# Kernel tuning notes

Measured on AMD Instinct MI355X. Metric: run time of the kernel, lower is better.

Reference implementation:

```python
import jax, jax.numpy as jnp
import numpy as np

MESH_POS = jnp.array([0.0, 0.0, -0.8], dtype=jnp.float32)
CAMERA_F = (248.0, 248.0)
CAMERA_C = (111.5, 111.5)


def _camera_mat(p):
    # p: [B, 5] camera metadata (azimuth deg, elevation deg, _, distance, _)
    d = jnp.pi / 180.0
    theta = p[:, 0] * d
    camy = p[:, 3] * jnp.sin(p[:, 1] * d)
    lens = p[:, 3] * jnp.cos(p[:, 1] * d)
    camx = lens * jnp.cos(theta)
    camz = lens * jnp.sin(theta)
    Z = jnp.stack([camx, camy, camz], -1)  # camera origin [B,3]
    Y = jnp.stack([camy * jnp.cos(theta + jnp.pi), lens,
                   camy * jnp.sin(theta + jnp.pi)], -1)
    X = jnp.cross(Y, Z)
    nrm = lambda v: v / jnp.linalg.norm(v, axis=-1, keepdims=True)
    cm = jnp.stack([nrm(X), nrm(Y), nrm(Z)], -2)  # [B,3,3] orthonormal rows
    return cm, Z


def _camera_trans(p, xyz):  # world -> camera: (xyz - O) @ cm.T
    cm, o = _camera_mat(p)
    return jnp.einsum('bij,bnj->bni', cm, xyz - o[:, None, :])


def _camera_trans_inv(p, xyz):  # camera -> world; cm orthonormal so inv(cm) = cm.T
    cm, o = _camera_mat(p)
    return jnp.einsum('bnj,bji->bni', xyz, cm) + o[:, None, :]


def _grid_sample(feat, gx, gy):
    # torch F.grid_sample: bilinear, padding_mode='zeros', align_corners=False
    B, C, H, W = feat.shape
    x = ((gx + 1.0) * W - 1.0) * 0.5  # [B,N] pixel coords
    y = ((gy + 1.0) * H - 1.0) * 0.5
    x0, y0 = jnp.floor(x), jnp.floor(y)
    x1, y1 = x0 + 1.0, y0 + 1.0
    wx1, wy1 = x - x0, y - y0
    wx0, wy0 = 1.0 - wx1, 1.0 - wy1
    flat = feat.reshape(B, C, H * W)

    def corner(xc, yc, wgt):
        xi = jnp.clip(xc, 0, W - 1).astype(jnp.int32)
        yi = jnp.clip(yc, 0, H - 1).astype(jnp.int32)
        valid = (xc >= 0) & (xc <= W - 1) & (yc >= 0) & (yc <= H - 1)
        v = jnp.take_along_axis(flat, (yi * W + xi)[:, None, :], axis=2)  # [B,C,N]
        return v * (wgt * valid)[:, None, :]

    out = (corner(x0, y0, wx0 * wy0) + corner(x1, y0, wx1 * wy0)
           + corner(x0, y1, wx0 * wy1) + corner(x1, y1, wx1 * wy1))
    return out.transpose(0, 2, 1)  # [B,N,C]


def setup_inputs() -> dict:
    key = jax.random.key(0)
    ks = jax.random.split(key, 7)
    B, V, N = 8, 3, 8192
    feat0 = jax.random.normal(ks[0], (V, B, 64, 56, 56), jnp.float32)
    feat1 = jax.random.normal(ks[1], (V, B, 128, 28, 28), jnp.float32)
    feat2 = jax.random.normal(ks[2], (V, B, 256, 14, 14), jnp.float32)
    inputs = jax.random.normal(ks[3], (B, N, 3), jnp.float32) * 0.2
    az = jax.random.uniform(ks[4], (B, V), minval=0.0, maxval=360.0)
    el = jax.random.uniform(ks[5], (B, V), minval=20.0, maxval=40.0)
    dist = jax.random.uniform(ks[6], (B, V), minval=0.8, maxval=1.2)
    poses = jnp.stack([az, el, jnp.zeros((B, V)), dist,
                       jnp.full((B, V), 25.0)], axis=-1).astype(jnp.float32)
    resolution = jnp.full((2,), 224, dtype=jnp.int32)
    return {"feat0": feat0, "feat1": feat1, "feat2": feat2,
            "inputs": inputs, "poses": poses, "resolution": resolution}


def reference(feat0, feat1, feat2, inputs, poses, resolution):
    res = resolution.astype(jnp.float32)
    half_res = (res - 1.0) * 0.5
    c_off0 = CAMERA_C[0] - half_res[0]
    c_off1 = CAMERA_C[1] - half_res[1]
    positions = inputs + MESH_POS
    point_origin = _camera_trans_inv(poses[:, 0], positions)
    V = poses.shape[1]
    feats_views = []
    for i in range(V):  # small fixed view count
        pos = _camera_trans(poses[:, i], point_origin)
        X, Y, Z = pos[..., 0], pos[..., 1], pos[..., 2]
        w = -CAMERA_F[0] * (X / Z) + c_off0  # bound=0 -> bound_val is identity
        h = CAMERA_F[1] * (Y / Z) + c_off1
        w = jnp.clip(w / half_res[0], -1.0, 1.0)
        h = jnp.clip(h / half_res[1], -1.0, 1.0)
        f = jnp.concatenate([_grid_sample(feat0[i], w, h),
                             _grid_sample(feat1[i], w, h),
                             _grid_sample(feat2[i], w, h)], axis=2)
        feats_views.append(f)
    outputs = jnp.stack(feats_views, axis=1)  # [B,V,N,448]
    out_max = jnp.max(outputs, axis=1)
    out_mean = jnp.mean(outputs, axis=1)
    out_std = jnp.std(outputs, axis=1, ddof=1)  # torch.std is unbiased
    return jnp.concatenate([inputs, out_max, out_mean, out_std], axis=2)
```

## Files before the change

### kernel.cpp

```cpp
#include <hip/hip_runtime.h>
#include <cstdint>
#include <cmath>


typedef float f32x2 __attribute__((ext_vector_type(2)));
typedef float f32x4 __attribute__((ext_vector_type(4)));
typedef _Float16 f16;
typedef _Float16 f16x2 __attribute__((ext_vector_type(2)));
typedef _Float16 f16x4 __attribute__((ext_vector_type(4)));

__device__ __forceinline__ void make_cam(const float* __restrict__ p, float* c) {
    const float d = 0.017453292519943295f;
    float theta = p[0] * d;
    float elr   = p[1] * d;
    float dist  = p[3];
    float st = sinf(theta), ct = cosf(theta);
    float se = sinf(elr),   ce = cosf(elr);
    float camy = dist * se;
    float lens = dist * ce;
    float camx = lens * ct;
    float camz = lens * st;
    float Zx = camx, Zy = camy, Zz = camz;
    float Yx = -camy * ct, Yy = lens, Yz = -camy * st;
    float Xx = Yy * Zz - Yz * Zy;
    float Xy = Yz * Zx - Yx * Zz;
    float Xz = Yx * Zy - Yy * Zx;
    float rx = 1.0f / sqrtf(Xx*Xx + Xy*Xy + Xz*Xz);
    float ry = 1.0f / sqrtf(Yx*Yx + Yy*Yy + Yz*Yz);
    float rz = 1.0f / sqrtf(Zx*Zx + Zy*Zy + Zz*Zz);
    c[0] = Xx*rx; c[1] = Xy*rx; c[2] = Xz*rx;
    c[3] = Yx*ry; c[4] = Yy*ry; c[5] = Yz*ry;
    c[6] = Zx*rz; c[7] = Zy*rz; c[8] = Zz*rz;
    c[9] = camx; c[10] = camy; c[11] = camz;
}

__global__ void setup_cams_kernel(const float* __restrict__ poses,
                                  const int* __restrict__ resolution,
                                  float* __restrict__ ws, int BV) {
    int t = blockIdx.x * blockDim.x + threadIdx.x;
    if (t == 0) {
        float h0 = ((float)resolution[0] - 1.0f) * 0.5f;
        float h1 = ((float)resolution[1] - 1.0f) * 0.5f;
        ws[0] = 111.5f - h0;
        ws[1] = 111.5f - h1;
        ws[2] = h0;
        ws[3] = h1;
    }
    if (t < BV) make_cam(poses + (size_t)t * 5, ws + 4 + (size_t)t * 12);
}

struct Corners {
    int p00, p10, p01, p11;
    float w00, w10, w01, w11;
};

__device__ __forceinline__ Corners mk_corners(float gx, float gy, int S) {
    float x = ((gx + 1.0f) * (float)S - 1.0f) * 0.5f;
    float y = ((gy + 1.0f) * (float)S - 1.0f) * 0.5f;
    float x0f = floorf(x), y0f = floorf(y);
    float wx1 = x - x0f, wy1 = y - y0f;
    float wx0 = 1.0f - wx1, wy0 = 1.0f - wy1;
    int x0 = (int)x0f, y0 = (int)y0f;
    int x1 = x0 + 1, y1 = y0 + 1;
    bool vx0 = (x0 >= 0) && (x0 <= S - 1);
    bool vx1 = (x1 >= 0) && (x1 <= S - 1);
    bool vy0 = (y0 >= 0) && (y0 <= S - 1);
    bool vy1 = (y1 >= 0) && (y1 <= S - 1);
    int xi0 = min(max(x0, 0), S - 1);
    int xi1 = min(max(x1, 0), S - 1);
    int yi0 = min(max(y0, 0), S - 1);
    int yi1 = min(max(y1, 0), S - 1);
    Corners c;
    c.p00 = yi0 * S + xi0;
    c.p10 = yi0 * S + xi1;
    c.p01 = yi1 * S + xi0;
    c.p11 = yi1 * S + xi1;
    c.w00 = wx0 * wy0 * ((vx0 && vy0) ? 1.0f : 0.0f);
    c.w10 = wx1 * wy0 * ((vx1 && vy0) ? 1.0f : 0.0f);
    c.w01 = wx0 * wy1 * ((vx0 && vy1) ? 1.0f : 0.0f);
    c.w11 = wx1 * wy1 * ((vx1 && vy1) ? 1.0f : 0.0f);
    return c;
}

__global__ __launch_bounds__(256) void prep_kernel(
    const float* __restrict__ f0, const float* __restrict__ f1,
    const float* __restrict__ f2, f16* __restrict__ t0, f16* __restrict__ t1,
    f16* __restrict__ t2, const float* __restrict__ inputs,
    const float* __restrict__ poses, const int* __restrict__ resolution,
    float* __restrict__ corn, int B, int N, int BV, int tgrid) {
    __shared__ float tile[32][33];
    const int bid = blockIdx.x;
    if (bid < tgrid) {
        const int nb0 = 98 * 2 * BV;
        const int nb1 = 25 * 4 * BV;
        const float* src; f16* dst; int C, P, tP, local;
        if (bid < nb0)            { src = f0; dst = t0; C = 64;  P = 3136; tP = 98; local = bid; }
        else if (bid < nb0 + nb1) { src = f1; dst = t1; C = 128; P = 784;  tP = 25; local = bid - nb0; }
        else                      { src = f2; dst = t2; C = 256; P = 196;  tP = 7;  local = bid - nb0 - nb1; }
        int per = tP * (C >> 5);
        int slice = local / per;
        int rem = local - slice * per;
        int cy = rem / tP;
        int cx = rem - cy * tP;
        const float* s = src + (size_t)slice * C * P;
        f16* d = dst + (size_t)slice * C * P;
        int p0 = cx * 32, c0 = cy * 32;
        int tx = threadIdx.x & 31, ty = threadIdx.x >> 5;
#pragma unroll
        for (int i = 0; i < 32; i += 8) {
            int c = c0 + ty + i, p = p0 + tx;
            if (p < P) tile[ty + i][tx] = s[(size_t)c * P + p];
        }
        __syncthreads();
#pragma unroll
        for (int i = 0; i < 32; i += 8) {
            int p = p0 + ty + i, c = c0 + tx;
            if (p < P) d[(size_t)p * C + c] = (f16)tile[tx][ty + i];
        }
    } else {
        int t = (bid - tgrid) * 256 + threadIdx.x;
        if (t >= B * N * 3) return;
        int point = t / 3;
        int v = t - point * 3;
        int b = point / N;

        float h0 = ((float)resolution[0] - 1.0f) * 0.5f;
        float h1 = ((float)resolution[1] - 1.0f) * 0.5f;
        float c_off0 = 111.5f - h0, c_off1 = 111.5f - h1;
        float inv_h0 = 1.0f / h0, inv_h1 = 1.0f / h1;

        float cm0[12], cmv[12];
        make_cam(poses + (size_t)(b * 3) * 5, cm0);
        make_cam(poses + (size_t)(b * 3 + v) * 5, cmv);

        const float* ip = inputs + (size_t)point * 3;
        const float px = ip[0], py = ip[1], pz = ip[2] - 0.8f;

        const float wx = px * cm0[0] + py * cm0[3] + pz * cm0[6] + cm0[9];
        const float wy = px * cm0[1] + py * cm0[4] + pz * cm0[7] + cm0[10];
        const float wz = px * cm0[2] + py * cm0[5] + pz * cm0[8] + cm0[11];

        float qx = wx - cmv[9], qy = wy - cmv[10], qz = wz - cmv[11];
        float Xc = cmv[0] * qx + cmv[1] * qy + cmv[2] * qz;
        float Yc = cmv[3] * qx + cmv[4] * qy + cmv[5] * qz;
        float Zc = cmv[6] * qx + cmv[7] * qy + cmv[8] * qz;
        float invZ = 1.0f / Zc;
        float wpix = -248.0f * (Xc * invZ) + c_off0;
        float hpix =  248.0f * (Yc * invZ) + c_off1;
        float gx = fminf(fmaxf(wpix * inv_h0, -1.0f), 1.0f);
        float gy = fminf(fmaxf(hpix * inv_h1, -1.0f), 1.0f);

        float* o = corn + (size_t)t * 24;
        const int S[3] = {56, 28, 14};
        const int CB[3] = {64 * 2, 128 * 2, 256 * 2};
#pragma unroll
        for (int lvl = 0; lvl < 3; ++lvl) {
            Corners cr = mk_corners(gx, gy, S[lvl]);
            o[lvl * 8 + 0] = __int_as_float(cr.p00 * CB[lvl]);
            o[lvl * 8 + 1] = __int_as_float(cr.p10 * CB[lvl]);
            o[lvl * 8 + 2] = __int_as_float(cr.p01 * CB[lvl]);
            o[lvl * 8 + 3] = __int_as_float(cr.p11 * CB[lvl]);
            o[lvl * 8 + 4] = cr.w00;
            o[lvl * 8 + 5] = cr.w10;
            o[lvl * 8 + 6] = cr.w01;
            o[lvl * 8 + 7] = cr.w11;
        }
    }
}

template <int VEC> struct VecOf;
template <> struct VecOf<1> { using T = float; };
template <> struct VecOf<2> { using T = f32x2; };
template <> struct VecOf<4> { using T = f32x4; };
template <int VEC> struct F16VecOf;
template <> struct F16VecOf<1> { using T = f16; };
template <> struct F16VecOf<2> { using T = f16x2; };
template <> struct F16VecOf<4> { using T = f16x4; };

template <int VEC>
__device__ __forceinline__ typename VecOf<VEC>::T
gather4(const f16* __restrict__ base, const int4 off, const float4 w, int lane) {
    using HV = typename F16VecOf<VEC>::T;
    using FV = typename VecOf<VEC>::T;
    const char* cb = (const char*)base;
    const int lo = lane * (VEC * 2);
    HV h00 = *(const HV*)(cb + off.x + lo);
    HV h10 = *(const HV*)(cb + off.y + lo);
    HV h01 = *(const HV*)(cb + off.z + lo);
    HV h11 = *(const HV*)(cb + off.w + lo);
    FV a00, a10, a01, a11;
    if constexpr (VEC == 1) {
        a00 = (float)h00; a10 = (float)h10; a01 = (float)h01; a11 = (float)h11;
    } else {
        a00 = __builtin_convertvector(h00, FV);
        a10 = __builtin_convertvector(h10, FV);
        a01 = __builtin_convertvector(h01, FV);
        a11 = __builtin_convertvector(h11, FV);
    }
    return w.x * a00 + w.y * a10 + w.z * a01 + w.w * a11;
}

template <typename VecT, int VEC>
__device__ __forceinline__ void stats3(VecT a, VecT b, VecT c,
                                       VecT* omx, VecT* ome, VecT* osd) {
    const float* pa = (const float*)&a;
    const float* pb = (const float*)&b;
    const float* pc = (const float*)&c;
    float* qx = (float*)omx; float* qe = (float*)ome; float* qs = (float*)osd;
#pragma unroll
    for (int j = 0; j < VEC; ++j) {
        float x = pa[j], y = pb[j], z = pc[j];
        float m = fmaxf(x, fmaxf(y, z));
        float mean = (x + y + z) * (1.0f / 3.0f);
        float dx = x - mean, dy = y - mean, dz = z - mean;
        float s = sqrtf((dx * dx + dy * dy + dz * dz) * 0.5f);
        qx[j] = m; qe[j] = mean; qs[j] = s;
    }
}

__global__ __launch_bounds__(256) void gproj_main_kernel(
    const f16* __restrict__ t0, const f16* __restrict__ t1,
    const f16* __restrict__ t2, const float* __restrict__ inputs,
    const float* __restrict__ corn, float* __restrict__ out, int B, int N) {
    __shared__ alignas(16) float sb[4 * 1347];
    const int wave = threadIdx.x >> 6;
    const int lane = threadIdx.x & 63;
    const int b = blockIdx.x % B;
    const int pb = (blockIdx.x / B) * 4;
    const int pib = pb + wave;
    const bool valid = pib < N;

    if (valid) {
        const int point = b * N + pib;
        const int pu = __builtin_amdgcn_readfirstlane(point);
        const int bu = __builtin_amdgcn_readfirstlane(b);
        const float* ip = inputs + (size_t)point * 3;

        float  v0[3];
        f32x2  v1[3];
        f32x4  v2[3];

#pragma unroll
        for (int v = 0; v < 3; ++v) {
            const float* cp = corn + (size_t)(pu * 3 + v) * 24;
            const int slice = v * B + bu;
            const f16* b0 = t0 + (size_t)slice * 64 * 3136;
            const f16* b1 = t1 + (size_t)slice * 128 * 784;
            const f16* b2 = t2 + (size_t)slice * 256 * 196;

            int4   o0 = *(const int4*)(cp);
            float4 w0 = *(const float4*)(cp + 4);
            int4   o1 = *(const int4*)(cp + 8);
            float4 w1 = *(const float4*)(cp + 12);
            int4   o2 = *(const int4*)(cp + 16);
            float4 w2 = *(const float4*)(cp + 20);

            v0[v] = gather4<1>(b0, o0, w0, lane);
            v1[v] = gather4<2>(b1, o1, w1, lane);
            v2[v] = gather4<4>(b2, o2, w2, lane);
        }

        float* row = sb + wave * 1347;
        if (lane < 3) row[lane] = ip[lane];
        {
            float mx = fmaxf(v0[0], fmaxf(v0[1], v0[2]));
            float mean = (v0[0] + v0[1] + v0[2]) * (1.0f / 3.0f);
            float dx = v0[0] - mean, dy = v0[1] - mean, dz = v0[2] - mean;
            float sd = sqrtf((dx * dx + dy * dy + dz * dz) * 0.5f);
            row[3 + lane] = mx;
            row[451 + lane] = mean;
            row[899 + lane] = sd;
        }
        {
            f32x2 mx, me, sd;
            stats3<f32x2, 2>(v1[0], v1[1], v1[2], &mx, &me, &sd);
            const int g = 64 + 2 * lane;
            row[3 + g] = mx.x;   row[3 + g + 1] = mx.y;
            row[451 + g] = me.x; row[451 + g + 1] = me.y;
            row[899 + g] = sd.x; row[899 + g + 1] = sd.y;
        }
        {
            f32x4 mx, me, sd;
            stats3<f32x4, 4>(v2[0], v2[1], v2[2], &mx, &me, &sd);
            const int g = 192 + 4 * lane;
#pragma unroll
            for (int e = 0; e < 4; ++e) {
                row[3 + g + e] = mx[e];
                row[451 + g + e] = me[e];
                row[899 + g + e] = sd[e];
            }
        }
    }
    __syncthreads();

    const int nvalid = min(N - pb, 4);
    const int len = nvalid * 1347;
    float* gout = out + (size_t)(b * N + pb) * 1347;
    const int len4 = len & ~3;
    for (int j = threadIdx.x * 4; j < len4; j += 1024) {
        f32x4 vv = *(const f32x4*)(sb + j);
        __builtin_nontemporal_store(vv, (f32x4*)(gout + j));
    }
    if ((len & 3) && threadIdx.x == 0) {
        for (int jj = len4; jj < len; ++jj) gout[jj] = sb[jj];
    }
}

template <int C, int VEC>
__device__ __forceinline__ typename VecOf<VEC>::T
samph(const f16* __restrict__ base, const Corners& cr, int lane) {
    using HV = typename F16VecOf<VEC>::T;
    using FV = typename VecOf<VEC>::T;
    const HV* r00 = (const HV*)(base + (size_t)cr.p00 * C);
    const HV* r10 = (const HV*)(base + (size_t)cr.p10 * C);
    const HV* r01 = (const HV*)(base + (size_t)cr.p01 * C);
    const HV* r11 = (const HV*)(base + (size_t)cr.p11 * C);
    HV h00 = r00[lane], h10 = r10[lane], h01 = r01[lane], h11 = r11[lane];
    FV a00, a10, a01, a11;
    if constexpr (VEC == 1) {
        a00 = (float)h00; a10 = (float)h10; a01 = (float)h01; a11 = (float)h11;
    } else {
        a00 = __builtin_convertvector(h00, FV);
        a10 = __builtin_convertvector(h10, FV);
        a01 = __builtin_convertvector(h01, FV);
        a11 = __builtin_convertvector(h11, FV);
    }
    return cr.w00 * a00 + cr.w10 * a10 + cr.w01 * a01 + cr.w11 * a11;
}

template <typename VecT, int VEC>
__device__ __forceinline__ void stats3_st(VecT a, VecT b, VecT c,
                                          float* pmx, float* pme, float* psd) {
    VecT mx, me, sd;
    stats3<VecT, VEC>(a, b, c, &mx, &me, &sd);
    *(VecT*)pmx = mx; *(VecT*)pme = me; *(VecT*)psd = sd;
}

__global__ __launch_bounds__(256) void gproj_fused_kernel(
    const f16* __restrict__ t0, const f16* __restrict__ t1,
    const f16* __restrict__ t2, const float* __restrict__ inputs,
    const float* __restrict__ cams, float* __restrict__ out, int B, int N) {
    const int wave = threadIdx.x >> 6;
    const int lane = threadIdx.x & 63;
    const int b = blockIdx.x % B;
    const int pib = (blockIdx.x / B) * 4 + wave;
    if (pib >= N) return;
    const int point = b * N + pib;

    const float c_off0 = cams[0], c_off1 = cams[1];
    const float inv_h0 = 1.0f / cams[2], inv_h1 = 1.0f / cams[3];
    const float* cam = cams + 4;

    const float* ip = inputs + (size_t)point * 3;
    const float px = ip[0], py = ip[1], pz = ip[2] - 0.8f;

    const float* m0 = cam + (size_t)(b * 3) * 12;
    const float wx = px * m0[0] + py * m0[3] + pz * m0[6] + m0[9];
    const float wy = px * m0[1] + py * m0[4] + pz * m0[7] + m0[10];
    const float wz = px * m0[2] + py * m0[5] + pz * m0[8] + m0[11];

    float  v0[3];
    f32x2  v1[3];
    f32x4  v2[3];

#pragma unroll
    for (int v = 0; v < 3; ++v) {
        const float* m = cam + (size_t)(b * 3 + v) * 12;
        float qx = wx - m[9], qy = wy - m[10], qz = wz - m[11];
        float Xc = m[0] * qx + m[1] * qy + m[2] * qz;
        float Yc = m[3] * qx + m[4] * qy + m[5] * qz;
        float Zc = m[6] * qx + m[7] * qy + m[8] * qz;
        float invZ = 1.0f / Zc;
        float wpix = -248.0f * (Xc * invZ) + c_off0;
        float hpix =  248.0f * (Yc * invZ) + c_off1;
        float gx = fminf(fmaxf(wpix * inv_h0, -1.0f), 1.0f);
        float gy = fminf(fmaxf(hpix * inv_h1, -1.0f), 1.0f);
        Corners cr0 = mk_corners(gx, gy, 56);
        Corners cr1 = mk_corners(gx, gy, 28);
        Corners cr2 = mk_corners(gx, gy, 14);
        const int slice = v * B + b;
        v0[v] = samph<64, 1>(t0 + (size_t)slice * 64 * 3136, cr0, lane);
        v1[v] = samph<128, 2>(t1 + (size_t)slice * 128 * 784, cr1, lane);
        v2[v] = samph<256, 4>(t2 + (size_t)slice * 256 * 196, cr2, lane);
    }

    float* op = out + (size_t)point * 1347;
    if (lane < 3) op[lane] = ip[lane];
    {
        float* basep = op + 3 + lane;
        float mx = fmaxf(v0[0], fmaxf(v0[1], v0[2]));
        float mean = (v0[0] + v0[1] + v0[2]) * (1.0f / 3.0f);
        float dx = v0[0] - mean, dy = v0[1] - mean, dz = v0[2] - mean;
        float sd = sqrtf((dx * dx + dy * dy + dz * dz) * 0.5f);
        basep[0] = mx; basep[448] = mean; basep[896] = sd;
    }
    {
        const int g = 64 + 2 * lane;
        stats3_st<f32x2, 2>(v1[0], v1[1], v1[2],
                            op + 3 + g, op + 451 + g, op + 899 + g);
    }
    {
        const int g = 192 + 4 * lane;
        stats3_st<f32x4, 4>(v2[0], v2[1], v2[2],
                            op + 3 + g, op + 451 + g, op + 899 + g);
    }
}

__device__ __forceinline__ float samp_cf(const float* __restrict__ base,
                                         const Corners& cr, int P, int c) {
    const float* bc = base + (size_t)c * P;
    return cr.w00 * bc[cr.p00] + cr.w10 * bc[cr.p10]
         + cr.w01 * bc[cr.p01] + cr.w11 * bc[cr.p11];
}

__global__ __launch_bounds__(256) void gproj_fallback_kernel(
    const float* __restrict__ f0, const float* __restrict__ f1,
    const float* __restrict__ f2, const float* __restrict__ inputs,
    const float* __restrict__ cams, float* __restrict__ out, int B, int N) {
    const int wave = threadIdx.x >> 6;
    const int lane = threadIdx.x & 63;
    const int point = blockIdx.x * 4 + wave;
    if (point >= B * N) return;
    const int b = point / N;

    const float c_off0 = cams[0], c_off1 = cams[1];
    const float inv_h0 = 1.0f / cams[2], inv_h1 = 1.0f / cams[3];
    const float* cam = cams + 4;

    const float* ip = inputs + (size_t)point * 3;
    const float px = ip[0], py = ip[1], pz = ip[2] - 0.8f;

    const float* m0 = cam + (size_t)(b * 3) * 12;
    const float wx = px * m0[0] + py * m0[3] + pz * m0[6] + m0[9];
    const float wy = px * m0[1] + py * m0[4] + pz * m0[7] + m0[10];
    const float wz = px * m0[2] + py * m0[5] + pz * m0[8] + m0[11];

    float vals[3][7];
#pragma unroll
    for (int v = 0; v < 3; ++v) {
        const float* m = cam + (size_t)(b * 3 + v) * 12;
        float qx = wx - m[9], qy = wy - m[10], qz = wz - m[11];
        float Xc = m[0] * qx + m[1] * qy + m[2] * qz;
        float Yc = m[3] * qx + m[4] * qy + m[5] * qz;
        float Zc = m[6] * qx + m[7] * qy + m[8] * qz;
        float invZ = 1.0f / Zc;
        float wpix = -248.0f * (Xc * invZ) + c_off0;
        float hpix =  248.0f * (Yc * invZ) + c_off1;
        float gx = fminf(fmaxf(wpix * inv_h0, -1.0f), 1.0f);
        float gy = fminf(fmaxf(hpix * inv_h1, -1.0f), 1.0f);
        Corners cr0 = mk_corners(gx, gy, 56);
        Corners cr1 = mk_corners(gx, gy, 28);
        Corners cr2 = mk_corners(gx, gy, 14);
        int slice = v * B + b;
        const float* b0 = f0 + (size_t)slice * 64 * 3136;
        const float* b1 = f1 + (size_t)slice * 128 * 784;
        const float* b2 = f2 + (size_t)slice * 256 * 196;
        vals[v][0] = samp_cf(b0, cr0, 3136, lane);
        vals[v][1] = samp_cf(b1, cr1, 784, lane);
        vals[v][2] = samp_cf(b1, cr1, 784, lane + 64);
        vals[v][3] = samp_cf(b2, cr2, 196, lane);
        vals[v][4] = samp_cf(b2, cr2, 196, lane + 64);
        vals[v][5] = samp_cf(b2, cr2, 196, lane + 128);
        vals[v][6] = samp_cf(b2, cr2, 196, lane + 192);
    }

    float* op = out + (size_t)point * 1347;
    if (lane < 3) op[lane] = ip[lane];
#pragma unroll
    for (int k = 0; k < 7; ++k) {
        float a = vals[0][k], bv = vals[1][k], cv = vals[2][k];
        float mx = fmaxf(a, fmaxf(bv, cv));
        float mean = (a + bv + cv) * (1.0f / 3.0f);
        float da = a - mean, db = bv - mean, dc = cv - mean;
        float sd = sqrtf((da * da + db * db + dc * dc) * 0.5f);
        int g = lane + 64 * k;
        op[3 + g] = mx;
        op[451 + g] = mean;
        op[899 + g] = sd;
    }
}

extern "C" void kernel_launch(void* const* d_in, const int* in_sizes, int n_in,
                              void* d_out, int out_size, void* d_ws, size_t ws_size,
                              hipStream_t stream) {
    const float* feat0 = (const float*)d_in[0];
    const float* feat1 = (const float*)d_in[1];
    const float* feat2 = (const float*)d_in[2];
    const float* inputs = (const float*)d_in[3];
    const float* poses = (const float*)d_in[4];
    const int* resolution = (const int*)d_in[5];
    float* out = (float*)d_out;
    float* ws = (float*)d_ws;

    const int V = 3;
    const int B = in_sizes[4] / (V * 5);
    const int N = in_sizes[3] / (B * 3);
    const int BV = B * V;
    const int total = B * N;

    const size_t cams_elems = 512;
    const size_t t0_elems = (size_t)BV * 64 * 3136;
    const size_t t1_elems = (size_t)BV * 128 * 784;
    const size_t t2_elems = (size_t)BV * 256 * 196;
    const size_t th_elems = t0_elems + t1_elems + t2_elems;
    const size_t corn_elems = (size_t)total * 3 * 24;
    const size_t need_mid  = cams_elems * sizeof(float) + th_elems * sizeof(f16);
    const size_t need_full = need_mid + corn_elems * sizeof(float);

    const int nbb = (N + 3) / 4;
    const int tgrid = BV * (98 * 2 + 25 * 4 + 7 * 8);

    if (ws_size >= need_full) {
        float* corn = ws + cams_elems;
        f16* t0 = (f16*)(corn + corn_elems);
        f16* t1 = t0 + t0_elems;
        f16* t2 = t1 + t1_elems;
        const int cgrid = (total * 3 + 255) / 256;
        prep_kernel<<<tgrid + cgrid, 256, 0, stream>>>(
            feat0, feat1, feat2, t0, t1, t2, inputs, poses, resolution,
            corn, B, N, BV, tgrid);
        gproj_main_kernel<<<B * nbb, 256, 0, stream>>>(t0, t1, t2, inputs, corn, out, B, N);
    } else if (ws_size >= need_mid) {
        setup_cams_kernel<<<1, 64, 0, stream>>>(poses, resolution, ws, BV);
        f16* t0 = (f16*)(ws + cams_elems);
        f16* t1 = t0 + t0_elems;
        f16* t2 = t1 + t1_elems;
        prep_kernel<<<tgrid, 256, 0, stream>>>(
            feat0, feat1, feat2, t0, t1, t2, inputs, poses, resolution,
            ws, B, N, BV, tgrid);
        gproj_fused_kernel<<<B * nbb, 256, 0, stream>>>(t0, t1, t2, inputs, ws, out, B, N);
    } else {
        setup_cams_kernel<<<1, 64, 0, stream>>>(poses, resolution, ws, BV);
        gproj_fallback_kernel<<<(total + 3) / 4, 256, 0, stream>>>(
            feat0, feat1, feat2, inputs, ws, out, B, N);
    }
}
```

Baseline: 95.46 us.

## Pack corner indices and weights to 16-bit and share camera matrices via LDS

The per-point corner record drops from 24 floats to 12 words. Pixel indices are stored as packed 16-bit values, scaled by a per-level shift at gather time, and bilinear weights are stored as fp16 pairs. The prep kernel now builds each camera matrix once per block in shared memory instead of twice per thread. This cuts write and read traffic on the intermediate corner buffer and removes redundant trig work, at the cost of fp16 precision in the interpolation weights. Blocks whose BV exceeds 256 would be unsupported, and the change relies on C times 2 bytes being a power of two.

```diff
diff --git a/kernel.cpp b/kernel.cpp
--- a/kernel.cpp
+++ b/kernel.cpp
@@ -82,13 +82,22 @@
     return c;
 }
 
+__device__ __forceinline__ unsigned pack_u16(int a, int b) {
+    return (unsigned)(a & 0xffff) | ((unsigned)b << 16);
+}
+__device__ __forceinline__ unsigned pack_f16(float a, float b) {
+    f16x2 h; h.x = (f16)a; h.y = (f16)b;
+    return __builtin_bit_cast(unsigned, h);
+}
+
 __global__ __launch_bounds__(256) void prep_kernel(
     const float* __restrict__ f0, const float* __restrict__ f1,
     const float* __restrict__ f2, f16* __restrict__ t0, f16* __restrict__ t1,
     f16* __restrict__ t2, const float* __restrict__ inputs,
     const float* __restrict__ poses, const int* __restrict__ resolution,
-    float* __restrict__ corn, int B, int N, int BV, int tgrid) {
+    unsigned* __restrict__ corn, int B, int N, int BV, int tgrid) {
     __shared__ float tile[32][33];
+    __shared__ float lds_cam[24 * 12];
     const int bid = blockIdx.x;
     if (bid < tgrid) {
         const int nb0 = 98 * 2 * BV;
@@ -118,6 +127,11 @@
             if (p < P) d[(size_t)p * C + c] = (f16)tile[tx][ty + i];
         }
     } else {
+        if (threadIdx.x < (unsigned)BV)
+            make_cam(poses + (size_t)threadIdx.x * 5,
+                     lds_cam + (size_t)threadIdx.x * 12);
+        __syncthreads();
+
         int t = (bid - tgrid) * 256 + threadIdx.x;
         if (t >= B * N * 3) return;
         int point = t / 3;
@@ -129,9 +143,8 @@
         float c_off0 = 111.5f - h0, c_off1 = 111.5f - h1;
         float inv_h0 = 1.0f / h0, inv_h1 = 1.0f / h1;
 
-        float cm0[12], cmv[12];
-        make_cam(poses + (size_t)(b * 3) * 5, cm0);
-        make_cam(poses + (size_t)(b * 3 + v) * 5, cmv);
+        const float* cm0 = lds_cam + (size_t)(b * 3) * 12;
+        const float* cmv = lds_cam + (size_t)(b * 3 + v) * 12;
 
         const float* ip = inputs + (size_t)point * 3;
         const float px = ip[0], py = ip[1], pz = ip[2] - 0.8f;
@@ -150,20 +163,17 @@
         float gx = fminf(fmaxf(wpix * inv_h0, -1.0f), 1.0f);
         float gy = fminf(fmaxf(hpix * inv_h1, -1.0f), 1.0f);
 
-        float* o = corn + (size_t)t * 24;
+        unsigned* o = corn + (size_t)t * 12;
         const int S[3] = {56, 28, 14};
-        const int CB[3] = {64 * 2, 128 * 2, 256 * 2};
 #pragma unroll
         for (int lvl = 0; lvl < 3; ++lvl) {
             Corners cr = mk_corners(gx, gy, S[lvl]);
-            o[lvl * 8 + 0] = __int_as_float(cr.p00 * CB[lvl]);
-            o[lvl * 8 + 1] = __int_as_float(cr.p10 * CB[lvl]);
-            o[lvl * 8 + 2] = __int_as_float(cr.p01 * CB[lvl]);
-            o[lvl * 8 + 3] = __int_as_float(cr.p11 * CB[lvl]);
-            o[lvl * 8 + 4] = cr.w00;
-            o[lvl * 8 + 5] = cr.w10;
-            o[lvl * 8 + 6] = cr.w01;
-            o[lvl * 8 + 7] = cr.w11;
+            uint4 slot;
+            slot.x = pack_u16(cr.p00, cr.p10);
+            slot.y = pack_u16(cr.p01, cr.p11);
+            slot.z = pack_f16(cr.w00, cr.w10);
+            slot.w = pack_f16(cr.w01, cr.w11);
+            *(uint4*)(o + lvl * 4) = slot;
         }
     }
 }
@@ -177,17 +187,25 @@
 template <> struct F16VecOf<2> { using T = f16x2; };
 template <> struct F16VecOf<4> { using T = f16x4; };
 
-template <int VEC>
+template <int VEC, int SHIFT>
 __device__ __forceinline__ typename VecOf<VEC>::T
-gather4(const f16* __restrict__ base, const int4 off, const float4 w, int lane) {
+gather4p(const f16* __restrict__ base, const uint4 pk, int lane) {
     using HV = typename F16VecOf<VEC>::T;
     using FV = typename VecOf<VEC>::T;
     const char* cb = (const char*)base;
     const int lo = lane * (VEC * 2);
-    HV h00 = *(const HV*)(cb + off.x + lo);
-    HV h10 = *(const HV*)(cb + off.y + lo);
-    HV h01 = *(const HV*)(cb + off.z + lo);
-    HV h11 = *(const HV*)(cb + off.w + lo);
+    const int o00 = (int)((pk.x & 0xffffu) << SHIFT) + lo;
+    const int o10 = (int)((pk.x >> 16) << SHIFT) + lo;
+    const int o01 = (int)((pk.y & 0xffffu) << SHIFT) + lo;
+    const int o11 = (int)((pk.y >> 16) << SHIFT) + lo;
+    HV h00 = *(const HV*)(cb + o00);
+    HV h10 = *(const HV*)(cb + o10);
+    HV h01 = *(const HV*)(cb + o01);
+    HV h11 = *(const HV*)(cb + o11);
+    f16x2 wlo = __builtin_bit_cast(f16x2, pk.z);
+    f16x2 whi = __builtin_bit_cast(f16x2, pk.w);
+    const float w00 = (float)wlo.x, w10 = (float)wlo.y;
+    const float w01 = (float)whi.x, w11 = (float)whi.y;
     FV a00, a10, a01, a11;
     if constexpr (VEC == 1) {
         a00 = (float)h00; a10 = (float)h10; a01 = (float)h01; a11 = (float)h11;
@@ -197,7 +215,7 @@
         a01 = __builtin_convertvector(h01, FV);
         a11 = __builtin_convertvector(h11, FV);
     }
-    return w.x * a00 + w.y * a10 + w.z * a01 + w.w * a11;
+    return w00 * a00 + w10 * a10 + w01 * a01 + w11 * a11;
 }
 
 template <typename VecT, int VEC>
@@ -221,7 +239,7 @@
 __global__ __launch_bounds__(256) void gproj_main_kernel(
     const f16* __restrict__ t0, const f16* __restrict__ t1,
     const f16* __restrict__ t2, const float* __restrict__ inputs,
-    const float* __restrict__ corn, float* __restrict__ out, int B, int N) {
+    const unsigned* __restrict__ corn, float* __restrict__ out, int B, int N) {
     __shared__ alignas(16) float sb[4 * 1347];
     const int wave = threadIdx.x >> 6;
     const int lane = threadIdx.x & 63;
@@ -242,22 +260,19 @@
 
 #pragma unroll
         for (int v = 0; v < 3; ++v) {
-            const float* cp = corn + (size_t)(pu * 3 + v) * 24;
+            const unsigned* cp = corn + (size_t)(pu * 3 + v) * 12;
             const int slice = v * B + bu;
             const f16* b0 = t0 + (size_t)slice * 64 * 3136;
             const f16* b1 = t1 + (size_t)slice * 128 * 784;
             const f16* b2 = t2 + (size_t)slice * 256 * 196;
 
-            int4   o0 = *(const int4*)(cp);
-            float4 w0 = *(const float4*)(cp + 4);
-            int4   o1 = *(const int4*)(cp + 8);
-            float4 w1 = *(const float4*)(cp + 12);
-            int4   o2 = *(const int4*)(cp + 16);
-            float4 w2 = *(const float4*)(cp + 20);
-
-            v0[v] = gather4<1>(b0, o0, w0, lane);
-            v1[v] = gather4<2>(b1, o1, w1, lane);
-            v2[v] = gather4<4>(b2, o2, w2, lane);
+            uint4 s0 = *(const uint4*)(cp);
+            uint4 s1 = *(const uint4*)(cp + 4);
+            uint4 s2 = *(const uint4*)(cp + 8);
+
+            v0[v] = gather4p<1, 7>(b0, s0, lane);
+            v1[v] = gather4p<2, 8>(b1, s1, lane);
+            v2[v] = gather4p<4, 9>(b2, s2, lane);
         }
 
         float* row = sb + wave * 1347;
@@ -503,15 +518,15 @@
     const size_t t1_elems = (size_t)BV * 128 * 784;
     const size_t t2_elems = (size_t)BV * 256 * 196;
     const size_t th_elems = t0_elems + t1_elems + t2_elems;
-    const size_t corn_elems = (size_t)total * 3 * 24;
+    const size_t corn_elems = (size_t)total * 3 * 12;
     const size_t need_mid  = cams_elems * sizeof(float) + th_elems * sizeof(f16);
-    const size_t need_full = need_mid + corn_elems * sizeof(float);
+    const size_t need_full = need_mid + corn_elems * sizeof(unsigned);
 
     const int nbb = (N + 3) / 4;
     const int tgrid = BV * (98 * 2 + 25 * 4 + 7 * 8);
 
     if (ws_size >= need_full) {
-        float* corn = ws + cams_elems;
+        unsigned* corn = (unsigned*)(ws + cams_elems);
         f16* t0 = (f16*)(corn + corn_elems);
         f16* t1 = t0 + t0_elems;
         f16* t2 = t1 + t1_elems;
@@ -527,7 +542,7 @@
         f16* t2 = t1 + t1_elems;
         prep_kernel<<<tgrid, 256, 0, stream>>>(
             feat0, feat1, feat2, t0, t1, t2, inputs, poses, resolution,
-            ws, B, N, BV, tgrid);
+            (unsigned*)ws, B, N, BV, tgrid);
         gproj_fused_kernel<<<B * nbb, 256, 0, stream>>>(t0, t1, t2, inputs, ws, out, B, N);
     } else {
         setup_cams_kernel<<<1, 64, 0, stream>>>(poses, resolution, ws, BV);
```

After: 88.13 us. 1.08x faster.
